# Kernel optimization log

Measured on AMD Instinct MI355X. Metric: run time of the kernel, lower is better.

Reference implementation:

```python
import jax, jax.numpy as jnp
from jax import lax
import numpy as np

C_IN = 64
C_OUT = 64
CQ = C_OUT // 8   # query/key channels
K = 5             # axial kernel length
RATIO = 0.7       # hybrid-norm mixing ratio
EPS = 1e-5
DN = ('NCHW', 'OIHW', 'NCHW')


def setup_inputs() -> dict:
    key = jax.random.key(0)
    ks = jax.random.split(key, 16)
    rn = lambda k, s, sc=0.05: jax.random.normal(k, s, dtype=jnp.float32) * sc
    return dict(
        x=jax.random.normal(ks[0], (4, C_IN, 256, 256), dtype=jnp.float32),
        hconv_w=rn(ks[1], (C_IN, 1, 1, K)), hconv_b=rn(ks[2], (C_IN,)),
        vconv_w=rn(ks[3], (C_IN, 1, K, 1)), vconv_b=rn(ks[4], (C_IN,)),
        pw_w=rn(ks[5], (C_OUT, C_IN)), pw_b=rn(ks[6], (C_OUT,)),
        bn_w=1.0 + rn(ks[7], (C_OUT,)), bn_b=rn(ks[8], (C_OUT,)),
        q_w=rn(ks[9], (CQ, C_OUT)), q_b=rn(ks[10], (CQ,)),
        k_w=rn(ks[11], (CQ, C_OUT)), k_b=rn(ks[12], (CQ,)),
        v_w=rn(ks[13], (C_OUT, C_OUT)), v_b=rn(ks[14], (C_OUT,)),
        gamma=rn(ks[15], (1,), 0.1),
    )


def reference(x, hconv_w, hconv_b, vconv_w, vconv_b, pw_w, pw_b,
              bn_w, bn_b, q_w, q_b, k_w, k_b, v_w, v_b, gamma):
    # ---- AxialDepthwiseConv: depthwise (1,K) + (K,1) + x, relu, pointwise ----
    h = lax.conv_general_dilated(x, hconv_w, (1, 1), [(0, 0), (K // 2, K // 2)],
                                 dimension_numbers=DN, feature_group_count=C_IN)
    h = h + hconv_b[:, None, None]
    v = lax.conv_general_dilated(x, vconv_w, (1, 1), [(K // 2, K // 2), (0, 0)],
                                 dimension_numbers=DN, feature_group_count=C_IN)
    v = v + vconv_b[:, None, None]
    a = jax.nn.relu(h + v + x)
    y = jnp.einsum('bchw,oc->bohw', a, pw_w) + pw_b[:, None, None]

    # ---- HybridNormalization: 0.7*InstanceNorm(no affine) + 0.3*BatchNorm(train) ----
    im = y.mean((2, 3), keepdims=True)
    iv = y.var((2, 3), keepdims=True)
    inn = (y - im) * lax.rsqrt(iv + EPS)
    bm = y.mean((0, 2, 3), keepdims=True)
    bv = y.var((0, 2, 3), keepdims=True)
    bnn = (y - bm) * lax.rsqrt(bv + EPS) * bn_w[:, None, None] + bn_b[:, None, None]
    y = RATIO * inn + (1.0 - RATIO) * bnn

    # ---- CrissCrossAttention ----
    q = jnp.einsum('bchw,oc->bohw', y, q_w) + q_b[:, None, None]   # (B,CQ,H,W)
    k = jnp.einsum('bchw,oc->bohw', y, k_w) + k_b[:, None, None]   # (B,CQ,H,W)
    val = jnp.einsum('bchw,oc->bohw', y, v_w) + v_b[:, None, None] # (B,C,H,W)

    # height (per column w): attn[b,w,j,i] = softmax_i( q[b,:,j,w] . k[b,:,i,w] )
    Ah = jax.nn.softmax(jnp.einsum('bcjw,bciw->bwji', q, k), axis=-1)
    # h_out[b,c,i,w] = sum_j val[b,c,j,w] * Ah[b,w,j,i]  (matches bmm(value, attn))
    h_out = jnp.einsum('bcjw,bwji->bciw', val, Ah)

    # width (per row h): attn[b,h,y,x] = softmax_x( q[b,:,h,y] . k[b,:,h,x] )
    Av = jax.nn.softmax(jnp.einsum('bchy,bchx->bhyx', q, k), axis=-1)
    v_out = jnp.einsum('bchy,bhyx->bchx', val, Av)

    out = gamma[0] * (h_out + v_out) + y

    # ---- MaxPool2d(2,2) ----
    down = lax.reduce_window(out, -jnp.inf, lax.max, (1, 1, 2, 2), (1, 1, 2, 2), 'VALID')
    return out, down
```

## Files before the change

kernel.cpp:

```cpp
#include <hip/hip_runtime.h>
#include <hip/hip_bf16.h>

#define Bn 4
#define Cc 64
#define CQn 8
#define Hh 256
#define Ww 256
#define PLANE 65536
#define LOG2E 1.4426950408889634f

typedef unsigned short ushortT;
typedef __attribute__((ext_vector_type(8))) unsigned short us8;
typedef __attribute__((ext_vector_type(4))) unsigned short us4;
typedef __attribute__((ext_vector_type(8))) __bf16 bf16x8;
typedef __attribute__((ext_vector_type(4))) float f32x4;

__device__ inline ushortT f2bf(float f) {
    __hip_bfloat16 h = __float2bfloat16(f);
    return *(ushortT*)&h;
}
__device__ inline float bf2f(ushortT u) {
    return __uint_as_float((unsigned)u << 16);
}
union BF8U { us8 u; bf16x8 b; uint4 w; };
__device__ inline us8 zero_us8() {
    BF8U z; z.w.x = 0; z.w.y = 0; z.w.z = 0; z.w.w = 0; return z.u;
}

__global__ void pack_weights_kernel(
    const float* __restrict__ pww, const float* __restrict__ qw,
    const float* __restrict__ kw, const float* __restrict__ vw,
    ushortT* __restrict__ pw_bf, ushortT* __restrict__ qk_bf,
    ushortT* __restrict__ vw_bf)
{
    int i = blockIdx.x * 256 + threadIdx.x;
    if (i < 64 * 64) pw_bf[i] = f2bf(pww[i]);
    if (i < 64 * 64) vw_bf[i] = f2bf(vw[i]);
    if (i < 8 * 64)  qk_bf[i] = f2bf(qw[i]);
    if (i >= 8 * 64 && i < 16 * 64) qk_bf[i] = f2bf(kw[i - 512]);
}

__global__ __launch_bounds__(256) void dw_kernel(
    const float* __restrict__ x,
    const float* __restrict__ hw, const float* __restrict__ hb,
    const float* __restrict__ vw, const float* __restrict__ vb,
    ushortT* __restrict__ aout)
{
    int blk = blockIdx.x;
    int bc = blk >> 4;
    int ht = blk & 15;
    int h0 = ht * 16;
    int c = bc & 63;
    int tid = threadIdx.x;
    __shared__ float rows[20][260];
    const float* xp = x + (size_t)bc * PLANE;
    #pragma unroll
    for (int i = 0; i < 20; ++i) {
        int hr = h0 - 2 + i;
        rows[i][tid + 2] = (hr >= 0 && hr < Hh) ? xp[hr * Ww + tid] : 0.f;
    }
    if (tid < 20) {
        rows[tid][0] = 0.f; rows[tid][1] = 0.f;
        rows[tid][258] = 0.f; rows[tid][259] = 0.f;
    }
    __syncthreads();

    float hw0 = hw[c * 5 + 0], hw1 = hw[c * 5 + 1], hw2 = hw[c * 5 + 2],
          hw3 = hw[c * 5 + 3], hw4 = hw[c * 5 + 4];
    float vw0 = vw[c * 5 + 0], vw1 = vw[c * 5 + 1], vw2 = vw[c * 5 + 2],
          vw3 = vw[c * 5 + 3], vw4 = vw[c * 5 + 4];
    float bias = hb[c] + vb[c];

    ushortT* op = aout + (size_t)bc * PLANE + h0 * Ww + tid;
    #pragma unroll
    for (int r = 0; r < 16; ++r) {
        float hs = hw0 * rows[r + 2][tid]     + hw1 * rows[r + 2][tid + 1]
                 + hw2 * rows[r + 2][tid + 2] + hw3 * rows[r + 2][tid + 3]
                 + hw4 * rows[r + 2][tid + 4];
        float vs = vw0 * rows[r][tid + 2]     + vw1 * rows[r + 1][tid + 2]
                 + vw2 * rows[r + 2][tid + 2] + vw3 * rows[r + 3][tid + 2]
                 + vw4 * rows[r + 4][tid + 2];
        float res = hs + vs + bias + rows[r + 2][tid + 2];
        op[r * Ww] = f2bf(fmaxf(res, 0.f));
    }
}

__global__ __launch_bounds__(256) void pw_mfma_kernel(
    const ushortT* __restrict__ a_bf, const ushortT* __restrict__ pw_bf,
    const float* __restrict__ pwb,
    float* __restrict__ y_raw, float* __restrict__ sums, float* __restrict__ sumsq)
{
    int blk = blockIdx.x;
    int b = blk >> 8;
    int t0 = (blk & 255) << 8;
    int tid = threadIdx.x, lane = tid & 63, wv = tid >> 6;
    int half = lane >> 4;
    int col = lane & 15;

    __shared__ ushortT ytile[256 * 74];

    {
        size_t base = (size_t)b * Cc * PLANE + t0 + tid;
        uint* wrow = (uint*)&ytile[tid * 74];
        #pragma unroll
        for (int c = 0; c < Cc; c += 2) {
            ushortT v0 = a_bf[base + (size_t)c * PLANE];
            ushortT v1 = a_bf[base + (size_t)(c + 1) * PLANE];
            wrow[c >> 1] = (uint)v0 | ((uint)v1 << 16);
        }
    }
    __syncthreads();

    int m0 = wv * 16;
    BF8U a0, a1;
    a0.u = *(const us8*)(pw_bf + (m0 + col) * 64 + half * 8);
    a1.u = *(const us8*)(pw_bf + (m0 + col) * 64 + 32 + half * 8);

    float bias[4], s[4], s2[4];
    #pragma unroll
    for (int r = 0; r < 4; ++r) {
        bias[r] = pwb[m0 + half * 4 + r];
        s[r] = 0.f; s2[r] = 0.f;
    }

    const uint* lw = (const uint*)ytile;
    #pragma unroll 4
    for (int t = 0; t < 16; ++t) {
        int rbase = (t * 16 + col) * 37 + half * 4;
        BF8U b0, b1;
        b0.w.x = lw[rbase];      b0.w.y = lw[rbase + 1];
        b0.w.z = lw[rbase + 2];  b0.w.w = lw[rbase + 3];
        b1.w.x = lw[rbase + 16]; b1.w.y = lw[rbase + 17];
        b1.w.z = lw[rbase + 18]; b1.w.w = lw[rbase + 19];
        f32x4 acc = (f32x4){0.f, 0.f, 0.f, 0.f};
        acc = __builtin_amdgcn_mfma_f32_16x16x32_bf16(a0.b, b0.b, acc, 0, 0, 0);
        acc = __builtin_amdgcn_mfma_f32_16x16x32_bf16(a1.b, b1.b, acc, 0, 0, 0);
        int pix = t * 16 + col;
        #pragma unroll
        for (int r = 0; r < 4; ++r) {
            int c = m0 + half * 4 + r;
            float v = acc[r] + bias[r];
            y_raw[(size_t)(b * Cc + c) * PLANE + t0 + pix] = v;
            s[r] += v; s2[r] += v * v;
        }
    }
    #pragma unroll
    for (int r = 0; r < 4; ++r) {
        #pragma unroll
        for (int d = 8; d > 0; d >>= 1) {
            s[r]  += __shfl_down(s[r], d, 16);
            s2[r] += __shfl_down(s2[r], d, 16);
        }
    }
    if (col == 0) {
        #pragma unroll
        for (int r = 0; r < 4; ++r) {
            int c = m0 + half * 4 + r;
            atomicAdd(&sums[b * Cc + c], s[r]);
            atomicAdd(&sumsq[b * Cc + c], s2[r]);
        }
    }
}

__global__ __launch_bounds__(256) void qkv_mfma_kernel(
    const float* __restrict__ y_raw,
    const float* __restrict__ sums, const float* __restrict__ sumsq,
    const float* __restrict__ bnw, const float* __restrict__ bnb,
    const ushortT* __restrict__ qk_bf, const float* __restrict__ qbias,
    const float* __restrict__ kbias,
    const ushortT* __restrict__ vw_bf, const float* __restrict__ vbias,
    ushortT* __restrict__ q, ushortT* __restrict__ k,
    ushortT* __restrict__ val)
{
    int blk = blockIdx.x;
    int b = blk >> 8;
    int t0 = (blk & 255) << 8;
    int tid = threadIdx.x, lane = tid & 63, wv = tid >> 6;
    int half = lane >> 4;
    int col = lane & 15;

    __shared__ ushortT ytile[256 * 74];
    __shared__ float alpha_s[64], beta_s[64];

    if (tid < 64) {
        int c = tid;
        float im[4], e2[4];
        float bm = 0.f, be2 = 0.f;
        #pragma unroll
        for (int bb = 0; bb < 4; ++bb) {
            im[bb] = sums[bb * Cc + c] * (1.f / 65536.f);
            e2[bb] = sumsq[bb * Cc + c] * (1.f / 65536.f);
            bm += im[bb]; be2 += e2[bb];
        }
        bm *= 0.25f; be2 *= 0.25f;
        float rsb = rsqrtf(be2 - bm * bm + 1e-5f);
        float wgt = bnw[c];
        float rsi = rsqrtf(e2[b] - im[b] * im[b] + 1e-5f);
        alpha_s[c] = 0.7f * rsi + 0.3f * rsb * wgt;
        beta_s[c]  = -0.7f * im[b] * rsi - 0.3f * bm * rsb * wgt + 0.3f * bnb[c];
    }
    __syncthreads();

    {
        size_t base = (size_t)b * Cc * PLANE + t0 + tid;
        uint* wrow = (uint*)&ytile[tid * 74];
        #pragma unroll
        for (int c = 0; c < Cc; c += 2) {
            float v0 = y_raw[base + (size_t)c * PLANE];
            float v1 = y_raw[base + (size_t)(c + 1) * PLANE];
            float n0 = alpha_s[c] * v0 + beta_s[c];
            float n1 = alpha_s[c + 1] * v1 + beta_s[c + 1];
            wrow[c >> 1] = (uint)f2bf(n0) | ((uint)f2bf(n1) << 16);
        }
    }
    __syncthreads();

    const uint* lw = (const uint*)ytile;

    {
        BF8U a0, a1;
        a0.u = *(const us8*)(qk_bf + col * 64 + half * 8);
        a1.u = *(const us8*)(qk_bf + col * 64 + 32 + half * 8);
        #pragma unroll
        for (int i = 0; i < 4; ++i) {
            int t = wv * 4 + i;
            int rbase = (t * 16 + col) * 37 + half * 4;
            BF8U b0, b1;
            b0.w.x = lw[rbase];      b0.w.y = lw[rbase + 1];
            b0.w.z = lw[rbase + 2];  b0.w.w = lw[rbase + 3];
            b1.w.x = lw[rbase + 16]; b1.w.y = lw[rbase + 17];
            b1.w.z = lw[rbase + 18]; b1.w.w = lw[rbase + 19];
            f32x4 acc = (f32x4){0.f, 0.f, 0.f, 0.f};
            acc = __builtin_amdgcn_mfma_f32_16x16x32_bf16(a0.b, b0.b, acc, 0, 0, 0);
            acc = __builtin_amdgcn_mfma_f32_16x16x32_bf16(a1.b, b1.b, acc, 0, 0, 0);
            int pix = t * 16 + col;
            #pragma unroll
            for (int r = 0; r < 4; ++r) {
                int row = half * 4 + r;
                if (row < 8)
                    q[(size_t)(b * CQn + row) * PLANE + t0 + pix] =
                        f2bf((acc[r] + qbias[row]) * LOG2E);
                else
                    k[(size_t)(b * CQn + row - 8) * PLANE + t0 + pix] = f2bf(acc[r] + kbias[row - 8]);
            }
        }
    }

    {
        int m0 = wv * 16;
        BF8U a0, a1;
        a0.u = *(const us8*)(vw_bf + (m0 + col) * 64 + half * 8);
        a1.u = *(const us8*)(vw_bf + (m0 + col) * 64 + 32 + half * 8);
        float bias[4];
        #pragma unroll
        for (int r = 0; r < 4; ++r) bias[r] = vbias[m0 + half * 4 + r];
        #pragma unroll 4
        for (int t = 0; t < 16; ++t) {
            int rbase = (t * 16 + col) * 37 + half * 4;
            BF8U b0, b1;
            b0.w.x = lw[rbase];      b0.w.y = lw[rbase + 1];
            b0.w.z = lw[rbase + 2];  b0.w.w = lw[rbase + 3];
            b1.w.x = lw[rbase + 16]; b1.w.y = lw[rbase + 17];
            b1.w.z = lw[rbase + 18]; b1.w.w = lw[rbase + 19];
            f32x4 acc = (f32x4){0.f, 0.f, 0.f, 0.f};
            acc = __builtin_amdgcn_mfma_f32_16x16x32_bf16(a0.b, b0.b, acc, 0, 0, 0);
            acc = __builtin_amdgcn_mfma_f32_16x16x32_bf16(a1.b, b1.b, acc, 0, 0, 0);
            int pix = t * 16 + col;
            #pragma unroll
            for (int r = 0; r < 4; ++r) {
                int c = m0 + half * 4 + r;
                val[(size_t)(b * Cc + c) * PLANE + t0 + pix] = f2bf(acc[r] + bias[r]);
            }
        }
    }
}

__global__ __launch_bounds__(256) void transpose_all_kernel(
    const ushortT* __restrict__ qb, ushortT* __restrict__ qT,
    const ushortT* __restrict__ kb, ushortT* __restrict__ kT,
    const ushortT* __restrict__ vb, ushortT* __restrict__ vT)
{
    int blk = blockIdx.x;
    int plane = blk >> 6;
    int tile = blk & 63;
    const ushortT* src; ushortT* dst;
    if (plane < 32)      { src = qb + (size_t)plane * PLANE;        dst = qT + (size_t)plane * PLANE; }
    else if (plane < 64) { src = kb + (size_t)(plane - 32) * PLANE; dst = kT + (size_t)(plane - 32) * PLANE; }
    else                 { src = vb + (size_t)(plane - 64) * PLANE; dst = vT + (size_t)(plane - 64) * PLANE; }
    int th = (tile >> 3) * 32;
    int tw = (tile & 7) * 32;
    __shared__ ushortT t[32][34];
    int lw = threadIdx.x & 31;
    int lh = threadIdx.x >> 5;
    #pragma unroll
    for (int i = 0; i < 4; ++i)
        t[lh + 8 * i][lw] = src[(th + lh + 8 * i) * Ww + tw + lw];
    __syncthreads();
    #pragma unroll
    for (int i = 0; i < 4; ++i)
        dst[(tw + lh + 8 * i) * Hh + th + lw] = t[lw][lh + 8 * i];
}

__global__ __launch_bounds__(256) void attn_kernel(
    const ushortT* __restrict__ q0, const ushortT* __restrict__ k0,
    const ushortT* __restrict__ v0, ushortT* __restrict__ o0,
    const ushortT* __restrict__ q1, const ushortT* __restrict__ k1,
    const ushortT* __restrict__ v1, ushortT* __restrict__ o1)
{
    int blk = blockIdx.x;
    int sel = blk >> 10;
    const ushortT* __restrict__ q   = sel ? q1 : q0;
    const ushortT* __restrict__ k   = sel ? k1 : k0;
    const ushortT* __restrict__ val = sel ? v1 : v0;
    ushortT* __restrict__ outp      = sel ? o1 : o0;
    int bblk = blk & 1023;
    int b = bblk >> 8;
    int r = bblk & 255;
    int tid = threadIdx.x;
    int lane = tid & 63;
    int wv = tid >> 6;
    int col = lane & 15;
    int quad = lane >> 4;

    __shared__ ushortT q_s[256 * 8];
    __shared__ ushortT k_s[256 * 8];
    __shared__ ushortT A_lds[2][4 * 256 * 8];
    __shared__ float mhat[256];
    __shared__ float shiftv[256];
    __shared__ float kred[32];

    size_t vbase = (size_t)b * Cc * PLANE + (size_t)r * Ww
                 + (size_t)(wv * 16 + col) * PLANE + quad * 8;
    BF8U afb[2];
    afb[0].u = *(const us8*)(val + vbase);

    size_t qkbase = (size_t)b * CQn * PLANE + (size_t)r * Ww + tid;
    float qf[8], ka[8];
    {
        BF8U qp, kp;
        #pragma unroll
        for (int c = 0; c < 8; ++c) {
            ushortT qv = q[qkbase + (size_t)c * PLANE];
            ushortT kv = k[qkbase + (size_t)c * PLANE];
            qp.u[c] = qv; kp.u[c] = kv;
            qf[c] = bf2f(qv);
            ka[c] = fabsf(bf2f(kv));
        }
        *(us8*)&q_s[tid * 8] = qp.u;
        *(us8*)&k_s[tid * 8] = kp.u;
    }
    #pragma unroll
    for (int d = 1; d < 64; d <<= 1)
        #pragma unroll
        for (int c = 0; c < 8; ++c)
            ka[c] = fmaxf(ka[c], __shfl_xor(ka[c], d));
    if (lane == 0)
        #pragma unroll
        for (int c = 0; c < 8; ++c) kred[wv * 8 + c] = ka[c];
    __syncthreads();

    {
        float mh = 0.f;
        #pragma unroll
        for (int c = 0; c < 8; ++c) {
            float km = fmaxf(fmaxf(kred[c], kred[8 + c]),
                             fmaxf(kred[16 + c], kred[24 + c]));
            mh += fabsf(qf[c]) * km;
        }
        mhat[tid] = mh;
    }
    __syncthreads();

    #pragma unroll
    for (int t = 0; t < 4; ++t) {
        int jt = wv * 4 + t;
        BF8U qa; qa.u = zero_us8();
        if (quad == 0) qa.u = *(const us8*)&q_s[(jt * 16 + col) * 8];
        float mh4[4];
        #pragma unroll
        for (int rr = 0; rr < 4; ++rr) mh4[rr] = mhat[jt * 16 + quad * 4 + rr];
        f32x4 ls = (f32x4){0.f, 0.f, 0.f, 0.f};
        for (int it = 0; it < 16; ++it) {
            BF8U kb;
            kb.u = *(const us8*)&k_s[(it * 16 + col) * 8];
            f32x4 sacc = (f32x4){0.f, 0.f, 0.f, 0.f};
            sacc = __builtin_amdgcn_mfma_f32_16x16x32_bf16(qa.b, kb.b, sacc, 0, 0, 0);
            #pragma unroll
            for (int rr = 0; rr < 4; ++rr)
                ls[rr] += __builtin_amdgcn_exp2f(sacc[rr] - mh4[rr]);
        }
        #pragma unroll
        for (int d = 1; d < 16; d <<= 1)
            #pragma unroll
            for (int rr = 0; rr < 4; ++rr)
                ls[rr] += __shfl_xor(ls[rr], d);
        if (col == 0)
            #pragma unroll
            for (int rr = 0; rr < 4; ++rr)
                shiftv[jt * 16 + quad * 4 + rr] = mh4[rr] + __builtin_amdgcn_logf(ls[rr]);
    }
    __syncthreads();

    BF8U kc[4];
    #pragma unroll
    for (int i = 0; i < 4; ++i)
        kc[i].u = *(const us8*)&k_s[((wv * 4 + i) * 16 + col) * 8];
    f32x4 acc[16];
    #pragma unroll
    for (int t = 0; t < 16; ++t) acc[t] = (f32x4){0.f, 0.f, 0.f, 0.f};

    auto compute_E = [&](int kslab, int buf) {
        #pragma unroll
        for (int jj2 = 0; jj2 < 2; ++jj2) {
            int jt = kslab * 2 + jj2;
            BF8U qa; qa.u = zero_us8();
            if (quad == 0) qa.u = *(const us8*)&q_s[(jt * 16 + col) * 8];
            float sh4[4];
            #pragma unroll
            for (int rr = 0; rr < 4; ++rr) sh4[rr] = shiftv[jt * 16 + quad * 4 + rr];
            #pragma unroll
            for (int i = 0; i < 4; ++i) {
                f32x4 sacc = (f32x4){0.f, 0.f, 0.f, 0.f};
                sacc = __builtin_amdgcn_mfma_f32_16x16x32_bf16(qa.b, kc[i].b, sacc, 0, 0, 0);
                us4 pk;
                #pragma unroll
                for (int rr = 0; rr < 4; ++rr)
                    pk[rr] = f2bf(__builtin_amdgcn_exp2f(sacc[rr] - sh4[rr]));
                int irow = (wv * 4 + i) * 16 + col;
                int jq = jj2 * 2 + (quad >> 1);
                *(us4*)&A_lds[buf][(jq * 256 + irow) * 8 + (quad & 1) * 4] = pk;
            }
        }
    };

    compute_E(0, 0);
    __syncthreads();

    #pragma unroll
    for (int ks = 0; ks < 8; ++ks) {
        int cur = ks & 1;
        if (ks < 7) {
            afb[cur ^ 1].u = *(const us8*)(val + vbase + (ks + 1) * 32);
            compute_E(ks + 1, cur ^ 1);
        }
        #pragma unroll
        for (int t = 0; t < 16; ++t) {
            BF8U bfr;
            bfr.u = *(const us8*)&A_lds[cur][(quad * 256 + t * 16 + col) * 8];
            acc[t] = __builtin_amdgcn_mfma_f32_16x16x32_bf16(afb[cur].b, bfr.b, acc[t], 0, 0, 0);
        }
        __syncthreads();
    }

    size_t obase = (size_t)b * Cc * PLANE + (size_t)r * Ww;
    #pragma unroll
    for (int t = 0; t < 16; ++t) {
        int i = t * 16 + col;
        #pragma unroll
        for (int rr = 0; rr < 4; ++rr) {
            int c = wv * 16 + quad * 4 + rr;
            outp[obase + (size_t)c * PLANE + i] = f2bf(acc[t][rr]);
        }
    }
}

__global__ __launch_bounds__(256) void final_kernel(
    const ushortT* __restrict__ houtT, const ushortT* __restrict__ hout0,
    const float* __restrict__ y_raw,
    const float* __restrict__ sums, const float* __restrict__ sumsq,
    const float* __restrict__ bnw, const float* __restrict__ bnb,
    const float* __restrict__ gamma,
    float* __restrict__ out, float* __restrict__ down)
{
    int blk = blockIdx.x;
    int tile = blk & 63;
    int bc = blk >> 6;
    int b = bc >> 6;
    int c = bc & 63;
    int th = (tile >> 3) * 32;
    int tw = (tile & 7) * 32;

    float im[4], e2[4];
    float bm = 0.f, be2 = 0.f;
    #pragma unroll
    for (int bb = 0; bb < 4; ++bb) {
        im[bb] = sums[bb * Cc + c] * (1.f / 65536.f);
        e2[bb] = sumsq[bb * Cc + c] * (1.f / 65536.f);
        bm += im[bb]; be2 += e2[bb];
    }
    bm *= 0.25f; be2 *= 0.25f;
    float rsb = rsqrtf(be2 - bm * bm + 1e-5f);
    float wgt = bnw[c];
    float rsi = rsqrtf(e2[b] - im[b] * im[b] + 1e-5f);
    float al = 0.7f * rsi + 0.3f * rsb * wgt;
    float bt = -0.7f * im[b] * rsi - 0.3f * bm * rsb * wgt + 0.3f * bnb[c];

    __shared__ float t[32][33];
    const ushortT* hT = houtT + (size_t)bc * PLANE;
    {
        int ww = threadIdx.x >> 3;
        int hh = (threadIdx.x & 7) * 4;
        us4 v4 = *(const us4*)(hT + (size_t)(tw + ww) * Hh + th + hh);
        t[hh + 0][ww] = __uint_as_float((unsigned)v4[0] << 16);
        t[hh + 1][ww] = __uint_as_float((unsigned)v4[1] << 16);
        t[hh + 2][ww] = __uint_as_float((unsigned)v4[2] << 16);
        t[hh + 3][ww] = __uint_as_float((unsigned)v4[3] << 16);
    }
    __syncthreads();
    float g = gamma[0];
    int qw_ = threadIdx.x & 15;
    int qh_ = threadIdx.x >> 4;
    const float* yb = y_raw + (size_t)bc * PLANE;
    const ushortT* hb = hout0 + (size_t)bc * PLANE;
    float* ob = out + (size_t)bc * PLANE;
    float mx = -1e30f;
    float2 res[2];
    #pragma unroll
    for (int i = 0; i < 2; ++i) {
        int hh = 2 * qh_ + i;
        int off = (th + hh) * Ww + tw + 2 * qw_;
        uint hv = *(const uint*)(hb + off);
        float2 y = *(const float2*)(yb + off);
        float y0 = al * y.x + bt;
        float y1 = al * y.y + bt;
        float o0 = g * (t[hh][2 * qw_]     + bf2f((ushortT)(hv & 0xffff))) + y0;
        float o1 = g * (t[hh][2 * qw_ + 1] + bf2f((ushortT)(hv >> 16)))   + y1;
        res[i] = make_float2(o0, o1);
        mx = fmaxf(mx, fmaxf(o0, o1));
    }
    #pragma unroll
    for (int i = 0; i < 2; ++i) {
        int off = (th + 2 * qh_ + i) * Ww + tw + 2 * qw_;
        *(float2*)(ob + off) = res[i];
    }
    down[(size_t)bc * 16384 + (th / 2 + qh_) * 128 + tw / 2 + qw_] = mx;
}

extern "C" void kernel_launch(void* const* d_in, const int* in_sizes, int n_in,
                              void* d_out, int out_size, void* d_ws, size_t ws_size,
                              hipStream_t stream)
{
    const float* x     = (const float*)d_in[0];
    const float* hw    = (const float*)d_in[1];
    const float* hb    = (const float*)d_in[2];
    const float* vw    = (const float*)d_in[3];
    const float* vb    = (const float*)d_in[4];
    const float* pww   = (const float*)d_in[5];
    const float* pwb   = (const float*)d_in[6];
    const float* bnw   = (const float*)d_in[7];
    const float* bnb   = (const float*)d_in[8];
    const float* qw    = (const float*)d_in[9];
    const float* qb    = (const float*)d_in[10];
    const float* kw    = (const float*)d_in[11];
    const float* kb    = (const float*)d_in[12];
    const float* vw2   = (const float*)d_in[13];
    const float* vb2   = (const float*)d_in[14];
    const float* gamma = (const float*)d_in[15];

    float* ws = (float*)d_ws;
    const size_t NP = (size_t)Bn * Cc * PLANE;
    const size_t NQ = (size_t)Bn * CQn * PLANE;
    float* y_raw  = ws;
    float* slotB  = ws + NP;
    float* slotC  = ws + 2 * NP;
    float* slotD  = ws + 2 * NP + NP / 2;
    float* ptr    = ws + 3 * NP;
    ushortT* qbuf = (ushortT*)ptr;
    ushortT* kbuf = qbuf + NQ;
    ushortT* qT   = kbuf + NQ;
    ushortT* kT   = qT + NQ;
    float* sums   = (float*)(kT + NQ);
    float* sumsq  = sums + 256;
    ushortT* pw_bf = (ushortT*)(sumsq + 256);
    ushortT* qk_bf = pw_bf + 64 * 64;
    ushortT* vw_bf = qk_bf + 16 * 64;

    ushortT* a_buf = (ushortT*)slotC;
    ushortT* valT  = (ushortT*)slotC;
    ushortT* valb  = (ushortT*)slotD;
    ushortT* hout0 = (ushortT*)slotB;
    ushortT* houtT = hout0 + NP;
    float* out  = (float*)d_out;
    float* down = out + NP;

    hipMemsetAsync(sums, 0, 512 * sizeof(float), stream);
    pack_weights_kernel<<<dim3(16), dim3(256), 0, stream>>>(
        pww, qw, kw, vw2, pw_bf, qk_bf, vw_bf);
    dw_kernel<<<dim3(Bn * Cc * 16), dim3(256), 0, stream>>>(
        x, hw, hb, vw, vb, a_buf);
    pw_mfma_kernel<<<dim3(Bn * 256), dim3(256), 0, stream>>>(
        a_buf, pw_bf, pwb, y_raw, sums, sumsq);
    qkv_mfma_kernel<<<dim3(Bn * 256), dim3(256), 0, stream>>>(
        y_raw, sums, sumsq, bnw, bnb, qk_bf, qb, kb, vw_bf, vb2,
        qbuf, kbuf, valb);
    transpose_all_kernel<<<dim3(320 * 64), dim3(256), 0, stream>>>(
        qbuf, qT, kbuf, kT, valb, valT);
    attn_kernel<<<dim3(2 * Bn * Hh), dim3(256), 0, stream>>>(
        qbuf, kbuf, valb, hout0, qT, kT, valT, houtT);
    final_kernel<<<dim3(Bn * Cc * 64), dim3(256), 0, stream>>>(
        houtT, hout0, y_raw, sums, sumsq, bnw, bnb, gamma, out, down);
}
```

Before: 364.3 us.

## Drop weight-pack kernel and single-buffer attention E tiles

Removes the separate weight-packing kernel launch; the pointwise and QKV kernels now read fp32 weights and convert them to bf16 in registers. The attention kernel's double-buffered exponent tile in LDS becomes a single buffer, with a sync between computing E and the MFMA accumulation. This saves one launch and halves that LDS allocation, which may raise occupancy, but it gives up the overlap between E computation and the value MFMAs.

```diff
diff --git a/kernel.cpp b/kernel.cpp
--- a/kernel.cpp
+++ b/kernel.cpp
@@ -25,19 +25,6 @@
 union BF8U { us8 u; bf16x8 b; uint4 w; };
 __device__ inline us8 zero_us8() {
     BF8U z; z.w.x = 0; z.w.y = 0; z.w.z = 0; z.w.w = 0; return z.u;
-}
-
-__global__ void pack_weights_kernel(
-    const float* __restrict__ pww, const float* __restrict__ qw,
-    const float* __restrict__ kw, const float* __restrict__ vw,
-    ushortT* __restrict__ pw_bf, ushortT* __restrict__ qk_bf,
-    ushortT* __restrict__ vw_bf)
-{
-    int i = blockIdx.x * 256 + threadIdx.x;
-    if (i < 64 * 64) pw_bf[i] = f2bf(pww[i]);
-    if (i < 64 * 64) vw_bf[i] = f2bf(vw[i]);
-    if (i < 8 * 64)  qk_bf[i] = f2bf(qw[i]);
-    if (i >= 8 * 64 && i < 16 * 64) qk_bf[i] = f2bf(kw[i - 512]);
 }
 
 __global__ __launch_bounds__(256) void dw_kernel(
@@ -86,7 +73,7 @@
 }
 
 __global__ __launch_bounds__(256) void pw_mfma_kernel(
-    const ushortT* __restrict__ a_bf, const ushortT* __restrict__ pw_bf,
+    const ushortT* __restrict__ a_bf, const float* __restrict__ pwwf,
     const float* __restrict__ pwb,
     float* __restrict__ y_raw, float* __restrict__ sums, float* __restrict__ sumsq)
 {
@@ -113,8 +100,14 @@
 
     int m0 = wv * 16;
     BF8U a0, a1;
-    a0.u = *(const us8*)(pw_bf + (m0 + col) * 64 + half * 8);
-    a1.u = *(const us8*)(pw_bf + (m0 + col) * 64 + 32 + half * 8);
+    {
+        const float* wr = pwwf + (m0 + col) * 64 + half * 8;
+        #pragma unroll
+        for (int e = 0; e < 8; ++e) {
+            a0.u[e] = f2bf(wr[e]);
+            a1.u[e] = f2bf(wr[32 + e]);
+        }
+    }
 
     float bias[4], s[4], s2[4];
     #pragma unroll
@@ -166,9 +159,9 @@
     const float* __restrict__ y_raw,
     const float* __restrict__ sums, const float* __restrict__ sumsq,
     const float* __restrict__ bnw, const float* __restrict__ bnb,
-    const ushortT* __restrict__ qk_bf, const float* __restrict__ qbias,
-    const float* __restrict__ kbias,
-    const ushortT* __restrict__ vw_bf, const float* __restrict__ vbias,
+    const float* __restrict__ qwf, const float* __restrict__ qbias,
+    const float* __restrict__ kwf, const float* __restrict__ kbias,
+    const float* __restrict__ vwf, const float* __restrict__ vbias,
     ushortT* __restrict__ q, ushortT* __restrict__ k,
     ushortT* __restrict__ val)
 {
@@ -218,9 +211,13 @@
     const uint* lw = (const uint*)ytile;
 
     {
+        const float* wr = (col < 8) ? (qwf + col * 64) : (kwf + (col - 8) * 64);
         BF8U a0, a1;
-        a0.u = *(const us8*)(qk_bf + col * 64 + half * 8);
-        a1.u = *(const us8*)(qk_bf + col * 64 + 32 + half * 8);
+        #pragma unroll
+        for (int e = 0; e < 8; ++e) {
+            a0.u[e] = f2bf(wr[half * 8 + e]);
+            a1.u[e] = f2bf(wr[32 + half * 8 + e]);
+        }
         #pragma unroll
         for (int i = 0; i < 4; ++i) {
             int t = wv * 4 + i;
@@ -249,8 +246,14 @@
     {
         int m0 = wv * 16;
         BF8U a0, a1;
-        a0.u = *(const us8*)(vw_bf + (m0 + col) * 64 + half * 8);
-        a1.u = *(const us8*)(vw_bf + (m0 + col) * 64 + 32 + half * 8);
+        {
+            const float* wr = vwf + (m0 + col) * 64 + half * 8;
+            #pragma unroll
+            for (int e = 0; e < 8; ++e) {
+                a0.u[e] = f2bf(wr[e]);
+                a1.u[e] = f2bf(wr[32 + e]);
+            }
+        }
         float bias[4];
         #pragma unroll
         for (int r = 0; r < 4; ++r) bias[r] = vbias[m0 + half * 4 + r];
@@ -324,7 +327,7 @@
 
     __shared__ ushortT q_s[256 * 8];
     __shared__ ushortT k_s[256 * 8];
-    __shared__ ushortT A_lds[2][4 * 256 * 8];
+    __shared__ ushortT A_lds[4 * 256 * 8];
     __shared__ float mhat[256];
     __shared__ float shiftv[256];
     __shared__ float kred[32];
@@ -409,10 +412,13 @@
     #pragma unroll
     for (int t = 0; t < 16; ++t) acc[t] = (f32x4){0.f, 0.f, 0.f, 0.f};
 
-    auto compute_E = [&](int kslab, int buf) {
+    #pragma unroll
+    for (int ks = 0; ks < 8; ++ks) {
+        if (ks < 7)
+            afb[(ks + 1) & 1].u = *(const us8*)(val + vbase + (ks + 1) * 32);
         #pragma unroll
         for (int jj2 = 0; jj2 < 2; ++jj2) {
-            int jt = kslab * 2 + jj2;
+            int jt = ks * 2 + jj2;
             BF8U qa; qa.u = zero_us8();
             if (quad == 0) qa.u = *(const us8*)&q_s[(jt * 16 + col) * 8];
             float sh4[4];
@@ -428,26 +434,15 @@
                     pk[rr] = f2bf(__builtin_amdgcn_exp2f(sacc[rr] - sh4[rr]));
                 int irow = (wv * 4 + i) * 16 + col;
                 int jq = jj2 * 2 + (quad >> 1);
-                *(us4*)&A_lds[buf][(jq * 256 + irow) * 8 + (quad & 1) * 4] = pk;
+                *(us4*)&A_lds[(jq * 256 + irow) * 8 + (quad & 1) * 4] = pk;
             }
         }
-    };
-
-    compute_E(0, 0);
-    __syncthreads();
-
-    #pragma unroll
-    for (int ks = 0; ks < 8; ++ks) {
-        int cur = ks & 1;
-        if (ks < 7) {
-            afb[cur ^ 1].u = *(const us8*)(val + vbase + (ks + 1) * 32);
-            compute_E(ks + 1, cur ^ 1);
-        }
+        __syncthreads();
         #pragma unroll
         for (int t = 0; t < 16; ++t) {
             BF8U bfr;
-            bfr.u = *(const us8*)&A_lds[cur][(quad * 256 + t * 16 + col) * 8];
-            acc[t] = __builtin_amdgcn_mfma_f32_16x16x32_bf16(afb[cur].b, bfr.b, acc[t], 0, 0, 0);
+            bfr.u = *(const us8*)&A_lds[(quad * 256 + t * 16 + col) * 8];
+            acc[t] = __builtin_amdgcn_mfma_f32_16x16x32_bf16(afb[ks & 1].b, bfr.b, acc[t], 0, 0, 0);
         }
         __syncthreads();
     }
@@ -571,9 +566,6 @@
     ushortT* kT   = qT + NQ;
     float* sums   = (float*)(kT + NQ);
     float* sumsq  = sums + 256;
-    ushortT* pw_bf = (ushortT*)(sumsq + 256);
-    ushortT* qk_bf = pw_bf + 64 * 64;
-    ushortT* vw_bf = qk_bf + 16 * 64;
 
     ushortT* a_buf = (ushortT*)slotC;
     ushortT* valT  = (ushortT*)slotC;
@@ -584,14 +576,12 @@
     float* down = out + NP;
 
     hipMemsetAsync(sums, 0, 512 * sizeof(float), stream);
-    pack_weights_kernel<<<dim3(16), dim3(256), 0, stream>>>(
-        pww, qw, kw, vw2, pw_bf, qk_bf, vw_bf);
     dw_kernel<<<dim3(Bn * Cc * 16), dim3(256), 0, stream>>>(
         x, hw, hb, vw, vb, a_buf);
     pw_mfma_kernel<<<dim3(Bn * 256), dim3(256), 0, stream>>>(
-        a_buf, pw_bf, pwb, y_raw, sums, sumsq);
+        a_buf, pww, pwb, y_raw, sums, sumsq);
     qkv_mfma_kernel<<<dim3(Bn * 256), dim3(256), 0, stream>>>(
-        y_raw, sums, sumsq, bnw, bnb, qk_bf, qb, kb, vw_bf, vb2,
+        y_raw, sums, sumsq, bnw, bnb, qw, qb, kw, kb, vw2, vb2,
         qbuf, kbuf, valb);
     transpose_all_kernel<<<dim3(320 * 64), dim3(256), 0, stream>>>(
         qbuf, qT, kbuf, kT, valb, valT);
```

New measurement: 358.2 us. About the same (-1.7%).
